# Kernel tuning notes

Measured on AMD Instinct MI355X. Metric: run time of the kernel, lower is better.

The kernel has to match this reference:

```python
import jax, jax.numpy as jnp
import numpy as np

N, E, B = 4096, 32768, 64
F_IN, E_FEAT, D, D3, G = 128, 64, 64, 64, 10
L = 3           # gc_count
SIG = 0.15      # prior_sig
LAMDA = 0.01    # DiffGroupNorm lambda
EPS = 1e-5      # BatchNorm eps


def setup_inputs() -> dict:
    key = jax.random.key(0)
    ks = jax.random.split(key, 24)
    u = lambda k, shape, s=0.02: jax.random.uniform(k, shape, jnp.float32, -s, s)
    return {
        "x": jax.random.normal(ks[0], (N, F_IN), jnp.float32),
        "edge_attr": jax.random.normal(ks[1], (E, E_FEAT), jnp.float32),
        "pre_W": u(ks[2], (F_IN, D)),
        "pre_b": u(ks[3], (D,)),
        "edge_w1": u(ks[4], (L, E_FEAT, D3), 0.1),
        "edge_b1": u(ks[5], (L, D3), 0.1),
        "edge_w2": u(ks[6], (L, D3, D * D), 0.05),
        "edge_b2": u(ks[7], (L, D * D), 0.05),
        "root_w": u(ks[8], (L, D, D), 0.1),
        "root_b": u(ks[9], (L, D), 0.1),
        "gru_wih": u(ks[10], (L, 3 * D, D), 0.1),
        "gru_whh": u(ks[11], (L, 3 * D, D), 0.1),
        "gru_bih": u(ks[12], (L, 3 * D), 0.1),
        "gru_bhh": u(ks[13], (L, 3 * D), 0.1),
        "gn_lin": u(ks[14], (L, D, G), 0.1),
        "gn_gamma": jnp.ones((L, G * D), jnp.float32),
        "gn_beta": jnp.zeros((L, G * D), jnp.float32),
        "post_W": u(ks[15], (D, D)),
        "post_b": u(ks[16], (D,)),
        "out_W": u(ks[17], (D, 1)),
        "out_b": u(ks[18], (1,)),
        "edge_index": jax.random.randint(ks[19], (2, E), 0, N),
        "batch": jnp.sort(jax.random.randint(ks[20], (N,), 0, B)),
    }


def _kld_det(W, b):
    # BayesLinear forward with sample=False: closed-form prior term
    logc = jnp.log(SIG * jnp.sqrt(2.0 * np.pi))
    return (0.5 * (W / SIG) ** 2 + logc).sum() + (0.5 * (b / SIG) ** 2 + logc).sum()


def _seg_mean(v, idx, num):
    s = jax.ops.segment_sum(v, idx, num_segments=num)
    c = jax.ops.segment_sum(jnp.ones((v.shape[0],), v.dtype), idx, num_segments=num)
    return s / jnp.clip(c, 1.0)[:, None]


def _gru_cell(m, h, wih, whh, bih, bhh):
    # torch GRU gate order: r, z, n
    gi = m @ wih.T + bih          # [N, 3D]
    gh = h @ whh.T + bhh
    i_r, i_z, i_n = jnp.split(gi, 3, axis=-1)
    h_r, h_z, h_n = jnp.split(gh, 3, axis=-1)
    r = jax.nn.sigmoid(i_r + h_r)
    z = jax.nn.sigmoid(i_z + h_z)
    n = jnp.tanh(i_n + r * h_n)
    return (1.0 - z) * n + z * h


def _diff_group_norm(m, lin, gamma, beta):
    # PyG DiffGroupNorm: x + lamda * sum_g s[:,g] * BN(s*x)
    s = jax.nn.softmax(m @ lin, axis=-1)           # [N, G]
    t = (s[:, :, None] * m[:, None, :]).reshape(m.shape[0], G * D)  # [N, G*D]
    mu = t.mean(axis=0)
    var = t.var(axis=0)                            # biased, as BatchNorm1d training
    tn = (t - mu) / jnp.sqrt(var + EPS) * gamma + beta
    return m + LAMDA * tn.reshape(m.shape[0], G, D).sum(axis=1)


def reference(x, edge_attr, pre_W, pre_b, edge_w1, edge_b1, edge_w2, edge_b2,
              root_w, root_b, gru_wih, gru_whh, gru_bih, gru_bhh,
              gn_lin, gn_gamma, gn_beta, post_W, post_b, out_W, out_b,
              edge_index, batch):
    src, dst = edge_index[0], edge_index[1]

    # pre FC (BayesLinear, sample=False) + relu
    out = jax.nn.relu(x @ pre_W + pre_b)
    tkl = _kld_det(pre_W, pre_b)
    prev = out
    h = out                                         # GRU hidden state

    for i in range(L):
        # edge-conditioned weights: MLP(edge_attr) -> [E, D, D]
        We = (jax.nn.relu(edge_attr @ edge_w1[i] + edge_b1[i]) @ edge_w2[i]
              + edge_b2[i]).reshape(E, D, D)
        msg = jnp.einsum('ef,efo->eo', out[src], We)        # gather + per-edge matmul
        agg = _seg_mean(msg, dst, N)                        # scatter-mean
        m = agg + out @ root_w[i] + root_b[i]               # NNConv root weight + bias
        m = _diff_group_norm(m, gn_lin[i], gn_gamma[i], gn_beta[i])
        m = jax.nn.relu(m)
        h = _gru_cell(m, h, gru_wih[i], gru_whh[i], gru_bih[i], gru_bhh[i])
        out = h + prev                                      # residual
        prev = out

    # early global_mean_pool over graphs
    pooled = _seg_mean(out, batch, B)                       # [B, D]
    p = jax.nn.relu(pooled @ post_W + post_b)
    tkl = tkl + _kld_det(post_W, post_b)
    y = p @ out_W + out_b                                   # [B, 1]
    tkl = tkl + _kld_det(out_W, out_b)
    return y.reshape(-1), tkl
```

## Files before the change

kernel.cpp:

```cpp
#include <hip/hip_runtime.h>
#include <math.h>

#define Nn 4096
#define Ee 32768
#define Bb 64
#define FINc 128
#define Dd 64
#define SIGf 0.15f
#define LAMf 0.01f
#define EPSf 1e-5f

typedef __attribute__((ext_vector_type(8))) short bf16x8;
typedef __attribute__((ext_vector_type(4))) float f32x4;

__device__ inline short f2bf(float f) {
  union { float f; unsigned u; } v; v.f = f;
  unsigned r = v.u + 0x7fffu + ((v.u >> 16) & 1u);
  return (short)(r >> 16);
}
__device__ inline bf16x8 pack8v(f32x4 a, f32x4 b) {
  bf16x8 r;
  r[0]=f2bf(a.x); r[1]=f2bf(a.y); r[2]=f2bf(a.z); r[3]=f2bf(a.w);
  r[4]=f2bf(b.x); r[5]=f2bf(b.y); r[6]=f2bf(b.z); r[7]=f2bf(b.w);
  return r;
}
__device__ inline float sigm(float x) { return 1.f / (1.f + expf(-x)); }

__global__ void k_tkl(const float* __restrict__ preW, const float* __restrict__ preb,
                      const float* __restrict__ postW, const float* __restrict__ postb,
                      const float* __restrict__ outW, const float* __restrict__ outb,
                      float* __restrict__ y) {
  int tid = threadIdx.x;
  const float logc = logf(SIGf * sqrtf(6.28318530717958647692f));
  const float c2 = 0.5f / (SIGf * SIGf);
  float acc = 0.f;
  for (int i = tid; i < FINc*Dd; i += 256) { float w = preW[i];  acc += c2*w*w + logc; }
  for (int i = tid; i < Dd; i += 256)      { float w = preb[i];  acc += c2*w*w + logc; }
  for (int i = tid; i < Dd*Dd; i += 256)   { float w = postW[i]; acc += c2*w*w + logc; }
  for (int i = tid; i < Dd; i += 256)      { float w = postb[i]; acc += c2*w*w + logc; }
  for (int i = tid; i < Dd; i += 256)      { float w = outW[i];  acc += c2*w*w + logc; }
  if (tid == 0)                            { float w = outb[0];  acc += c2*w*w + logc; }
  __shared__ float red[256];
  red[tid] = acc; __syncthreads();
  for (int s = 128; s > 0; s >>= 1) { if (tid < s) red[tid] += red[tid+s]; __syncthreads(); }
  if (tid == 0) y[Bb] = red[0];
}

__global__ void k_count(const int* __restrict__ dst, float* __restrict__ cnt) {
  int e = blockIdx.x * 256 + threadIdx.x;
  if (e < Ee) atomicAdd(&cnt[dst[e]], 1.0f);
}

__global__ void k_prep(const float* __restrict__ w1, const float* __restrict__ w2,
                       const float* __restrict__ b2, const float* __restrict__ rootw,
                       const float* __restrict__ gwih, const float* __restrict__ gwhh,
                       const float* __restrict__ preW,
                       short* __restrict__ w1T, short* __restrict__ b2T,
                       short* __restrict__ w2T, short* __restrict__ rootwT,
                       short* __restrict__ gwihB, short* __restrict__ gwhhB,
                       short* __restrict__ preWT) {
  int idx = blockIdx.x * 256 + threadIdx.x;
  if (idx < 3*64*64*64) {
    int f = idx & 63, o = (idx >> 6) & 63, h = (idx >> 12) & 63, l = idx >> 18;
    w2T[idx] = f2bf(w2[(((l*64 + h)*64 + f) << 6) + o]);
  }
  if (idx < 3*64*64) {
    int f = idx & 63, h = (idx >> 6) & 63, l = idx >> 12;
    w1T[idx] = f2bf(w1[l*4096 + f*64 + h]);
    b2T[idx] = f2bf(b2[l*4096 + f*64 + h]);
    rootwT[idx] = f2bf(rootw[l*4096 + f*64 + h]);
  }
  if (idx < 3*192*64) {
    gwihB[idx] = f2bf(gwih[idx]);
    gwhhB[idx] = f2bf(gwhh[idx]);
  }
  if (idx < 64*128) {
    int k = idx & 127, d = idx >> 7;
    preWT[idx] = f2bf(preW[k*64 + d]);
  }
}

__global__ __launch_bounds__(256) void k_pre(const float* __restrict__ x,
                                             const short* __restrict__ preWT,
                                             const float* __restrict__ preb,
                                             float* __restrict__ out, float* __restrict__ h) {
  const int tid = threadIdx.x, lane = tid & 63, wave = tid >> 6;
  const int m15 = lane & 15, kq = lane >> 4;
  const int nb = blockIdx.x * 32;
  const f32x4 zero4 = {0.f,0.f,0.f,0.f};
  const int d = wave*16 + m15;
  bf16x8 bfr[4];
  #pragma unroll
  for (int c = 0; c < 4; ++c)
    bfr[c] = *(const bf16x8*)(preWT + d*128 + c*32 + kq*8);
  #pragma unroll
  for (int t = 0; t < 2; ++t) {
    const float* xp = x + (size_t)(nb + t*16 + m15)*128 + kq*8;
    f32x4 p = zero4;
    #pragma unroll
    for (int c = 0; c < 4; ++c) {
      bf16x8 a = pack8v(*(const f32x4*)(xp + c*32), *(const f32x4*)(xp + c*32 + 4));
      p = __builtin_amdgcn_mfma_f32_16x16x32_bf16(a, bfr[c], p, 0, 0, 0);
    }
    float bv = preb[d];
    #pragma unroll
    for (int r = 0; r < 4; ++r) {
      int node = nb + t*16 + kq*4 + r;
      float v = fmaxf(p[r] + bv, 0.f);
      out[node*64 + d] = v;
      h[node*64 + d] = v;
    }
  }
}

__global__ __launch_bounds__(256) void k_msg(
    const float* __restrict__ out, const float* __restrict__ edge_attr,
    const short* __restrict__ w1T, const float* __restrict__ b1,
    const short* __restrict__ w2T, const short* __restrict__ b2T,
    const int* __restrict__ src, const int* __restrict__ dst,
    float* __restrict__ agg) {
  __shared__ __align__(16) float hidT[64*68];
  __shared__ int srcv[64];
  __shared__ int dstv[64];

  const int tid  = threadIdx.x;
  const int lane = tid & 63;
  const int wave = tid >> 6;
  const int m15  = lane & 15;
  const int kq   = lane >> 4;
  const int ebase = blockIdx.x * 64;

  if (tid < 64) { srcv[tid] = src[ebase + tid]; dstv[tid] = dst[ebase + tid]; }
  __syncthreads();

  const f32x4 zero4 = {0.f, 0.f, 0.f, 0.f};

  bf16x8 sfrag[4][2];
  #pragma unroll
  for (int t = 0; t < 4; ++t) {
    int node = srcv[t*16 + m15];
    const float* sp = out + node*64 + kq*8;
    #pragma unroll
    for (int ks = 0; ks < 2; ++ks) {
      f32x4 a = *(const f32x4*)(sp + ks*32);
      f32x4 b = *(const f32x4*)(sp + ks*32 + 4);
      sfrag[t][ks] = pack8v(a, b);
    }
  }

  {
    const short* wp = w1T + (wave*16 + m15)*64 + kq*8;
    bf16x8 bw0 = *(const bf16x8*)(wp);
    bf16x8 bw1 = *(const bf16x8*)(wp + 32);
    float b1v = b1[wave*16 + m15];
    #pragma unroll
    for (int t = 0; t < 4; ++t) {
      const float* ep = edge_attr + (size_t)(ebase + t*16 + m15)*64 + kq*8;
      bf16x8 a0 = pack8v(*(const f32x4*)(ep),      *(const f32x4*)(ep + 4));
      bf16x8 a1 = pack8v(*(const f32x4*)(ep + 32), *(const f32x4*)(ep + 36));
      f32x4 p = __builtin_amdgcn_mfma_f32_16x16x32_bf16(a0, bw0, zero4, 0, 0, 0);
      p = __builtin_amdgcn_mfma_f32_16x16x32_bf16(a1, bw1, p, 0, 0, 0);
      f32x4 v;
      v.x = fmaxf(p.x + b1v, 0.f); v.y = fmaxf(p.y + b1v, 0.f);
      v.z = fmaxf(p.z + b1v, 0.f); v.w = fmaxf(p.w + b1v, 0.f);
      *(f32x4*)(hidT + (wave*16 + m15)*68 + t*16 + kq*4) = v;
    }
  }
  __syncthreads();

  f32x4 acc[4] = {zero4, zero4, zero4, zero4};
  const short* w2base = w2T + (wave*16 + m15)*64 + kq*8;
  const short* b2base = b2T + (wave*16 + m15)*64 + kq*8;
  bf16x8 bc0 = *(const bf16x8*)(w2base);
  bf16x8 bc1 = *(const bf16x8*)(w2base + 32);
  for (int h = 0; h < 64; ++h) {
    const short* nb = (h < 63) ? (w2base + (h + 1)*4096) : b2base;
    bf16x8 pb0 = *(const bf16x8*)(nb);
    bf16x8 pb1 = *(const bf16x8*)(nb + 32);
    #pragma unroll
    for (int t = 0; t < 4; ++t) {
      f32x4 p = __builtin_amdgcn_mfma_f32_16x16x32_bf16(sfrag[t][0], bc0, zero4, 0, 0, 0);
      p = __builtin_amdgcn_mfma_f32_16x16x32_bf16(sfrag[t][1], bc1, p, 0, 0, 0);
      f32x4 hv = *(const f32x4*)(hidT + h*68 + t*16 + kq*4);
      acc[t].x += hv.x * p.x; acc[t].y += hv.y * p.y;
      acc[t].z += hv.z * p.z; acc[t].w += hv.w * p.w;
    }
    bc0 = pb0; bc1 = pb1;
  }
  #pragma unroll
  for (int t = 0; t < 4; ++t) {
    f32x4 p = __builtin_amdgcn_mfma_f32_16x16x32_bf16(sfrag[t][0], bc0, zero4, 0, 0, 0);
    p = __builtin_amdgcn_mfma_f32_16x16x32_bf16(sfrag[t][1], bc1, p, 0, 0, 0);
    acc[t].x += p.x; acc[t].y += p.y; acc[t].z += p.z; acc[t].w += p.w;
  }

  const int o = wave*16 + m15;
  #pragma unroll
  for (int t = 0; t < 4; ++t) {
    #pragma unroll
    for (int r = 0; r < 4; ++r) {
      int e = t*16 + kq*4 + r;
      atomicAdd(&agg[dstv[e]*64 + o], acc[t][r]);
    }
  }
}

__global__ __launch_bounds__(256) void k_m_fused(
    const float* __restrict__ agg, const float* __restrict__ cnt,
    const float* __restrict__ out, const short* __restrict__ rootwT,
    const float* __restrict__ rootb, const float* __restrict__ gnlin,
    float* __restrict__ m, float* __restrict__ sbuf, float* __restrict__ stats) {
  __shared__ float msh[64*65];
  __shared__ float lgsh[64*12];
  __shared__ float ssh[64*16];
  const int tid = threadIdx.x, lane = tid & 63, wave = tid >> 6;
  const int m15 = lane & 15, kq = lane >> 4;
  const int nb = blockIdx.x * 64;
  const f32x4 zero4 = {0.f,0.f,0.f,0.f};
  const int d = wave*16 + m15;

  bf16x8 b0 = *(const bf16x8*)(rootwT + d*64 + kq*8);
  bf16x8 b1 = *(const bf16x8*)(rootwT + d*64 + 32 + kq*8);
  float rbv = rootb[d];
  #pragma unroll
  for (int t = 0; t < 4; ++t) {
    const float* sp = out + (size_t)(nb + t*16 + m15)*64 + kq*8;
    bf16x8 a0 = pack8v(*(const f32x4*)(sp),      *(const f32x4*)(sp + 4));
    bf16x8 a1 = pack8v(*(const f32x4*)(sp + 32), *(const f32x4*)(sp + 36));
    f32x4 p = __builtin_amdgcn_mfma_f32_16x16x32_bf16(a0, b0, zero4, 0, 0, 0);
    p = __builtin_amdgcn_mfma_f32_16x16x32_bf16(a1, b1, p, 0, 0, 0);
    #pragma unroll
    for (int r = 0; r < 4; ++r) {
      int ln = t*16 + kq*4 + r;
      int node = nb + ln;
      float mv = agg[node*64 + d] / fmaxf(cnt[node], 1.f) + rbv + p[r];
      m[node*64 + d] = mv;
      msh[ln*65 + d] = mv;
    }
  }
  __syncthreads();

  for (int c = tid; c < 1024; c += 256) {
    int n = c >> 4, g = c & 15;
    if (g < 10) {
      float lg = 0.f;
      #pragma unroll 8
      for (int k = 0; k < 64; ++k) lg += msh[n*65 + k] * gnlin[k*10 + g];
      lgsh[n*12 + g] = lg;
    }
  }
  __syncthreads();
  for (int c = tid; c < 1024; c += 256) {
    int n = c >> 4, g = c & 15;
    if (g < 10) {
      float mx = -1e30f;
      #pragma unroll
      for (int gg = 0; gg < 10; ++gg) mx = fmaxf(mx, lgsh[n*12 + gg]);
      float sum = 0.f;
      #pragma unroll
      for (int gg = 0; gg < 10; ++gg) sum += expf(lgsh[n*12 + gg] - mx);
      float sv = expf(lgsh[n*12 + g] - mx) / sum;
      sbuf[(nb + n)*16 + g] = sv;
      ssh[n*16 + g] = sv;
    }
  }
  __syncthreads();
  for (int c = tid; c < 640; c += 256) {
    int g = c >> 6, dd = c & 63;
    float a1 = 0.f, a2 = 0.f;
    #pragma unroll 8
    for (int n = 0; n < 64; ++n) {
      float t = ssh[n*16 + g] * msh[n*65 + dd];
      a1 += t; a2 += t*t;
    }
    atomicAdd(&stats[c], a1);
    atomicAdd(&stats[640 + c], a2);
  }
}

__global__ __launch_bounds__(256) void k_gru(
    const float* __restrict__ m, const float* __restrict__ sbuf,
    const float* __restrict__ stats, const float* __restrict__ gamma,
    const float* __restrict__ beta, const short* __restrict__ gwihB,
    const short* __restrict__ gwhhB, const float* __restrict__ bih,
    const float* __restrict__ bhh, float* __restrict__ h,
    float* __restrict__ out) {
  __shared__ __align__(16) float mrsh[32*68];
  __shared__ float igsh[640];
  __shared__ float Bsh[64];
  __shared__ float ssh[512];
  const int tid = threadIdx.x, lane = tid & 63, wave = tid >> 6;
  const int m15 = lane & 15, kq = lane >> 4;
  const int nb = blockIdx.x * 32;
  const f32x4 zero4 = {0.f,0.f,0.f,0.f};
  const float invN = 1.f / (float)Nn;

  if (tid < 64) {
    float bacc = 0.f;
    #pragma unroll
    for (int g = 0; g < 10; ++g) {
      int c = g*64 + tid;
      float mu = stats[c] * invN;
      float var = stats[640 + c] * invN - mu*mu;
      float ig = (1.0f / sqrtf(var + EPSf)) * gamma[c];
      igsh[c] = ig;
      bacc += beta[c] - mu * ig;
    }
    Bsh[tid] = bacc;
  }
  if (tid < 512) ssh[tid] = sbuf[nb*16 + tid];
  __syncthreads();

  for (int idx = tid; idx < 2048; idx += 256) {
    int n = idx >> 6, dd = idx & 63;
    float mv = m[(nb + n)*64 + dd];
    float SA = 0.f;
    #pragma unroll
    for (int g = 0; g < 10; ++g) SA += ssh[n*16 + g] * igsh[g*64 + dd];
    mrsh[n*68 + dd] = fmaxf(mv * (1.f + LAMf*SA) + LAMf*Bsh[dd], 0.f);
  }
  __syncthreads();

  bf16x8 mrf[2][2], hf[2][2];
  #pragma unroll
  for (int t = 0; t < 2; ++t) {
    const float* mp = mrsh + (t*16 + m15)*68 + kq*8;
    const float* hp = h + (size_t)(nb + t*16 + m15)*64 + kq*8;
    #pragma unroll
    for (int ks = 0; ks < 2; ++ks) {
      mrf[t][ks] = pack8v(*(const f32x4*)(mp + ks*32), *(const f32x4*)(mp + ks*32 + 4));
      hf[t][ks]  = pack8v(*(const f32x4*)(hp + ks*32), *(const f32x4*)(hp + ks*32 + 4));
    }
  }
  const int d = wave*16 + m15;
  f32x4 gi[2][3], gh[2][3];
  #pragma unroll
  for (int p = 0; p < 3; ++p) {
    int j = p*64 + d;
    bf16x8 bi0 = *(const bf16x8*)(gwihB + j*64 + kq*8);
    bf16x8 bi1 = *(const bf16x8*)(gwihB + j*64 + 32 + kq*8);
    bf16x8 bh0 = *(const bf16x8*)(gwhhB + j*64 + kq*8);
    bf16x8 bh1 = *(const bf16x8*)(gwhhB + j*64 + 32 + kq*8);
    #pragma unroll
    for (int t = 0; t < 2; ++t) {
      f32x4 a = __builtin_amdgcn_mfma_f32_16x16x32_bf16(mrf[t][0], bi0, zero4, 0, 0, 0);
      gi[t][p] = __builtin_amdgcn_mfma_f32_16x16x32_bf16(mrf[t][1], bi1, a, 0, 0, 0);
      f32x4 b = __builtin_amdgcn_mfma_f32_16x16x32_bf16(hf[t][0], bh0, zero4, 0, 0, 0);
      gh[t][p] = __builtin_amdgcn_mfma_f32_16x16x32_bf16(hf[t][1], bh1, b, 0, 0, 0);
    }
  }
  float bir = bih[d],      bhr = bhh[d];
  float biz = bih[64 + d], bhz = bhh[64 + d];
  float bin = bih[128 + d], bhn = bhh[128 + d];
  __syncthreads();
  #pragma unroll
  for (int t = 0; t < 2; ++t) {
    #pragma unroll
    for (int r = 0; r < 4; ++r) {
      int node = nb + t*16 + kq*4 + r;
      float rr = sigm(gi[t][0][r] + bir + gh[t][0][r] + bhr);
      float z  = sigm(gi[t][1][r] + biz + gh[t][1][r] + bhz);
      float nn = tanhf(gi[t][2][r] + bin + rr * (gh[t][2][r] + bhn));
      float hv = h[node*64 + d];
      float hn = (1.f - z) * nn + z * hv;
      h[node*64 + d] = hn;
      out[node*64 + d] = hn + out[node*64 + d];
    }
  }
}

__global__ void k_pool(const float* __restrict__ out, const int* __restrict__ batch,
                       float* __restrict__ pooled, float* __restrict__ pcnt) {
  int idx = blockIdx.x * 256 + threadIdx.x;
  int n = idx >> 6, d = idx & 63;
  int b = batch[n];
  atomicAdd(&pooled[b*64 + d], out[idx]);
  if (d == 0) atomicAdd(&pcnt[b], 1.f);
}

__global__ void k_final(const float* __restrict__ pooled, const float* __restrict__ pcnt,
                        const float* __restrict__ postW, const float* __restrict__ postb,
                        const float* __restrict__ outW, const float* __restrict__ outb,
                        float* __restrict__ y) {
  int b = blockIdx.x, d = threadIdx.x;
  __shared__ float pl[64];
  float c = fmaxf(pcnt[b], 1.f);
  pl[d] = pooled[b*64 + d] / c;
  __syncthreads();
  float acc = postb[d];
  #pragma unroll 8
  for (int k = 0; k < 64; ++k) acc += pl[k] * postW[k*64 + d];
  acc = fmaxf(acc, 0.f);
  float v = acc * outW[d];
  #pragma unroll
  for (int off = 32; off > 0; off >>= 1) v += __shfl_down(v, off, 64);
  if (d == 0) y[b] = v + outb[0];
}

extern "C" void kernel_launch(void* const* d_in, const int* in_sizes, int n_in,
                              void* d_out, int out_size, void* d_ws, size_t ws_size,
                              hipStream_t stream) {
  (void)in_sizes; (void)n_in; (void)out_size; (void)ws_size;
  const float* x        = (const float*)d_in[0];
  const float* edge_attr= (const float*)d_in[1];
  const float* preW     = (const float*)d_in[2];
  const float* preb     = (const float*)d_in[3];
  const float* ew1      = (const float*)d_in[4];
  const float* eb1      = (const float*)d_in[5];
  const float* ew2      = (const float*)d_in[6];
  const float* eb2      = (const float*)d_in[7];
  const float* rootw    = (const float*)d_in[8];
  const float* rootb    = (const float*)d_in[9];
  const float* gwih     = (const float*)d_in[10];
  const float* gwhh     = (const float*)d_in[11];
  const float* gbih     = (const float*)d_in[12];
  const float* gbhh     = (const float*)d_in[13];
  const float* gnlin    = (const float*)d_in[14];
  const float* gngamma  = (const float*)d_in[15];
  const float* gnbeta   = (const float*)d_in[16];
  const float* postW    = (const float*)d_in[17];
  const float* postb    = (const float*)d_in[18];
  const float* outW     = (const float*)d_in[19];
  const float* outb     = (const float*)d_in[20];
  const int*   eidx     = (const int*)d_in[21];
  const int*   batch    = (const int*)d_in[22];
  const int* src = eidx;
  const int* dst = eidx + Ee;
  float* y = (float*)d_out;

  float* ws     = (float*)d_ws;
  float* out    = ws;
  float* hbuf   = out    + Nn*64;
  float* mbuf   = hbuf   + Nn*64;
  float* sbuf   = mbuf   + Nn*64;
  float* agg    = sbuf   + Nn*16;
  float* stats  = agg    + Nn*64;
  float* cnt    = stats  + 2048;
  float* pooled = cnt    + Nn;
  float* pcnt   = pooled + Nn;
  float* bfbase = pcnt   + 64;
  short* w1T    = (short*)bfbase;
  short* b2T    = w1T    + 3*4096;
  short* w2T    = b2T    + 3*4096;
  short* rootwT = w2T    + 3*262144;
  short* gwihB  = rootwT + 3*4096;
  short* gwhhB  = gwihB  + 3*12288;
  short* preWT  = gwhhB  + 3*12288;

  hipMemsetAsync(cnt, 0, (Nn + Nn + 64)*sizeof(float), stream);

  k_prep<<<3072, 256, 0, stream>>>(ew1, ew2, eb2, rootw, gwih, gwhh, preW,
                                   w1T, b2T, w2T, rootwT, gwihB, gwhhB, preWT);
  k_tkl<<<1, 256, 0, stream>>>(preW, preb, postW, postb, outW, outb, y);
  k_count<<<Ee/256, 256, 0, stream>>>(dst, cnt);
  k_pre<<<Nn/32, 256, 0, stream>>>(x, preWT, preb, out, hbuf);

  for (int i = 0; i < 3; ++i) {
    hipMemsetAsync(agg, 0, (Nn*64 + 2048)*sizeof(float), stream);
    k_msg<<<Ee/64, 256, 0, stream>>>(out, edge_attr,
                                     w1T + i*4096, eb1 + i*64,
                                     w2T + i*262144, b2T + i*4096,
                                     src, dst, agg);
    k_m_fused<<<Nn/64, 256, 0, stream>>>(agg, cnt, out, rootwT + i*4096,
                                         rootb + i*64, gnlin + i*640, mbuf, sbuf, stats);
    k_gru<<<Nn/32, 256, 0, stream>>>(mbuf, sbuf, stats, gngamma + i*640, gnbeta + i*640,
                                     gwihB + i*12288, gwhhB + i*12288,
                                     gbih + i*192, gbhh + i*192, hbuf, out);
  }

  k_pool<<<Nn*64/256, 256, 0, stream>>>(out, batch, pooled, pcnt);
  k_final<<<Bb, 64, 0, stream>>>(pooled, pcnt, postW, postb, outW, outb, y);
}
```

Baseline: 379.1 us.

## Merge setup kernels, split k_msg hidden loop across waves, fuse pool and zeroing

Folds weight conversion, KL term, edge/pool counting into one k_setup launch, with w2 transposed through shared memory for coalescing. k_msg now uses 512 threads: two wave groups each process half of the 64 hidden units and reduce through LDS before the atomics, doubling wave parallelism per block. The per-layer agg memset is replaced by zeroing agg inside k_m_fused after it is read, stats get per-layer slices, and the global mean pool atomics are fused into the last k_gru. These cut launch count and memset overhead and raise occupancy in the dominant message kernel, at the cost of extra LDS reduction and syncs.

```diff
diff --git a/kernel.cpp b/kernel.cpp
--- a/kernel.cpp
+++ b/kernel.cpp
@@ -26,57 +26,73 @@
 }
 __device__ inline float sigm(float x) { return 1.f / (1.f + expf(-x)); }
 
-__global__ void k_tkl(const float* __restrict__ preW, const float* __restrict__ preb,
-                      const float* __restrict__ postW, const float* __restrict__ postb,
-                      const float* __restrict__ outW, const float* __restrict__ outb,
-                      float* __restrict__ y) {
-  int tid = threadIdx.x;
-  const float logc = logf(SIGf * sqrtf(6.28318530717958647692f));
-  const float c2 = 0.5f / (SIGf * SIGf);
-  float acc = 0.f;
-  for (int i = tid; i < FINc*Dd; i += 256) { float w = preW[i];  acc += c2*w*w + logc; }
-  for (int i = tid; i < Dd; i += 256)      { float w = preb[i];  acc += c2*w*w + logc; }
-  for (int i = tid; i < Dd*Dd; i += 256)   { float w = postW[i]; acc += c2*w*w + logc; }
-  for (int i = tid; i < Dd; i += 256)      { float w = postb[i]; acc += c2*w*w + logc; }
-  for (int i = tid; i < Dd; i += 256)      { float w = outW[i];  acc += c2*w*w + logc; }
-  if (tid == 0)                            { float w = outb[0];  acc += c2*w*w + logc; }
-  __shared__ float red[256];
-  red[tid] = acc; __syncthreads();
-  for (int s = 128; s > 0; s >>= 1) { if (tid < s) red[tid] += red[tid+s]; __syncthreads(); }
-  if (tid == 0) y[Bb] = red[0];
-}
-
-__global__ void k_count(const int* __restrict__ dst, float* __restrict__ cnt) {
-  int e = blockIdx.x * 256 + threadIdx.x;
-  if (e < Ee) atomicAdd(&cnt[dst[e]], 1.0f);
-}
-
-__global__ void k_prep(const float* __restrict__ w1, const float* __restrict__ w2,
-                       const float* __restrict__ b2, const float* __restrict__ rootw,
-                       const float* __restrict__ gwih, const float* __restrict__ gwhh,
-                       const float* __restrict__ preW,
-                       short* __restrict__ w1T, short* __restrict__ b2T,
-                       short* __restrict__ w2T, short* __restrict__ rootwT,
-                       short* __restrict__ gwihB, short* __restrict__ gwhhB,
-                       short* __restrict__ preWT) {
-  int idx = blockIdx.x * 256 + threadIdx.x;
-  if (idx < 3*64*64*64) {
-    int f = idx & 63, o = (idx >> 6) & 63, h = (idx >> 12) & 63, l = idx >> 18;
-    w2T[idx] = f2bf(w2[(((l*64 + h)*64 + f) << 6) + o]);
-  }
-  if (idx < 3*64*64) {
-    int f = idx & 63, h = (idx >> 6) & 63, l = idx >> 12;
-    w1T[idx] = f2bf(w1[l*4096 + f*64 + h]);
-    b2T[idx] = f2bf(b2[l*4096 + f*64 + h]);
-    rootwT[idx] = f2bf(rootw[l*4096 + f*64 + h]);
-  }
-  if (idx < 3*192*64) {
-    gwihB[idx] = f2bf(gwih[idx]);
-    gwhhB[idx] = f2bf(gwhh[idx]);
-  }
-  if (idx < 64*128) {
-    int k = idx & 127, d = idx >> 7;
-    preWT[idx] = f2bf(preW[k*64 + d]);
+__global__ __launch_bounds__(256) void k_setup(
+    const float* __restrict__ w1, const float* __restrict__ w2,
+    const float* __restrict__ b2, const float* __restrict__ rootw,
+    const float* __restrict__ gwih, const float* __restrict__ gwhh,
+    const float* __restrict__ preW,
+    const float* __restrict__ preb, const float* __restrict__ postW,
+    const float* __restrict__ postb, const float* __restrict__ outW,
+    const float* __restrict__ outb,
+    const int* __restrict__ dst, const int* __restrict__ batch,
+    short* __restrict__ w1T, short* __restrict__ b2T,
+    short* __restrict__ w2T, short* __restrict__ rootwT,
+    short* __restrict__ gwihB, short* __restrict__ gwhhB,
+    short* __restrict__ preWT,
+    float* __restrict__ cnt, float* __restrict__ pcnt, float* __restrict__ y) {
+  const int b = blockIdx.x, tid = threadIdx.x;
+  if (b < 192) {
+    __shared__ float tile[64*65];
+    const int l = b >> 6, h = b & 63;
+    const float* srcp = w2 + (size_t)(l*64 + h)*4096;
+    #pragma unroll
+    for (int it = 0; it < 16; ++it) {
+      int j = tid + 256*it;
+      tile[(j >> 6)*65 + (j & 63)] = srcp[j];
+    }
+    __syncthreads();
+    short* dstp = w2T + (size_t)(l*64 + h)*4096;
+    #pragma unroll
+    for (int it = 0; it < 16; ++it) {
+      int j = tid + 256*it;
+      int o = j >> 6, f = j & 63;
+      dstp[j] = f2bf(tile[f*65 + o]);
+    }
+  } else if (b < 200) {
+    int base = (b - 192)*256 + tid;
+    for (int idx = base; idx < 12288; idx += 2048) {
+      int l = idx >> 12, r = idx & 4095;
+      int f = r & 63, c = r >> 6;
+      w1T[idx]    = f2bf(w1[l*4096 + f*64 + c]);
+      b2T[idx]    = f2bf(b2[l*4096 + f*64 + c]);
+      rootwT[idx] = f2bf(rootw[l*4096 + f*64 + c]);
+    }
+    for (int idx = base; idx < 36864; idx += 2048) {
+      gwihB[idx] = f2bf(gwih[idx]);
+      gwhhB[idx] = f2bf(gwhh[idx]);
+    }
+    for (int idx = base; idx < 8192; idx += 2048) {
+      int k = idx & 127, d = idx >> 7;
+      preWT[idx] = f2bf(preW[k*64 + d]);
+    }
+  } else if (b < 328) {
+    int e = (b - 200)*256 + tid;
+    atomicAdd(&cnt[dst[e]], 1.0f);
+    if (e < Nn) atomicAdd(&pcnt[batch[e]], 1.0f);
+  } else {
+    const float logc = logf(SIGf * sqrtf(6.28318530717958647692f));
+    const float c2 = 0.5f / (SIGf * SIGf);
+    float acc = 0.f;
+    for (int i = tid; i < FINc*Dd; i += 256) { float w = preW[i];  acc += c2*w*w + logc; }
+    for (int i = tid; i < Dd; i += 256)      { float w = preb[i];  acc += c2*w*w + logc; }
+    for (int i = tid; i < Dd*Dd; i += 256)   { float w = postW[i]; acc += c2*w*w + logc; }
+    for (int i = tid; i < Dd; i += 256)      { float w = postb[i]; acc += c2*w*w + logc; }
+    for (int i = tid; i < Dd; i += 256)      { float w = outW[i];  acc += c2*w*w + logc; }
+    if (tid == 0)                            { float w = outb[0];  acc += c2*w*w + logc; }
+    __shared__ float red[256];
+    red[tid] = acc; __syncthreads();
+    for (int s = 128; s > 0; s >>= 1) { if (tid < s) red[tid] += red[tid+s]; __syncthreads(); }
+    if (tid == 0) y[Bb] = red[0];
   }
 }
 
@@ -113,7 +129,7 @@
   }
 }
 
-__global__ __launch_bounds__(256) void k_msg(
+__global__ __launch_bounds__(512, 4) void k_msg(
     const float* __restrict__ out, const float* __restrict__ edge_attr,
     const short* __restrict__ w1T, const float* __restrict__ b1,
     const short* __restrict__ w2T, const short* __restrict__ b2T,
@@ -125,7 +141,9 @@
 
   const int tid  = threadIdx.x;
   const int lane = tid & 63;
-  const int wave = tid >> 6;
+  const int w    = tid >> 6;
+  const int ow   = w & 3;
+  const int hh   = w >> 2;
   const int m15  = lane & 15;
   const int kq   = lane >> 4;
   const int ebase = blockIdx.x * 64;
@@ -139,22 +157,20 @@
   #pragma unroll
   for (int t = 0; t < 4; ++t) {
     int node = srcv[t*16 + m15];
-    const float* sp = out + node*64 + kq*8;
-    #pragma unroll
-    for (int ks = 0; ks < 2; ++ks) {
-      f32x4 a = *(const f32x4*)(sp + ks*32);
-      f32x4 b = *(const f32x4*)(sp + ks*32 + 4);
-      sfrag[t][ks] = pack8v(a, b);
-    }
+    const float* sp = out + (size_t)node*64 + kq*8;
+    #pragma unroll
+    for (int ks = 0; ks < 2; ++ks)
+      sfrag[t][ks] = pack8v(*(const f32x4*)(sp + ks*32), *(const f32x4*)(sp + ks*32 + 4));
   }
 
   {
-    const short* wp = w1T + (wave*16 + m15)*64 + kq*8;
+    const short* wp = w1T + (ow*16 + m15)*64 + kq*8;
     bf16x8 bw0 = *(const bf16x8*)(wp);
     bf16x8 bw1 = *(const bf16x8*)(wp + 32);
-    float b1v = b1[wave*16 + m15];
-    #pragma unroll
-    for (int t = 0; t < 4; ++t) {
+    float b1v = b1[ow*16 + m15];
+    #pragma unroll
+    for (int tt = 0; tt < 2; ++tt) {
+      int t = hh*2 + tt;
       const float* ep = edge_attr + (size_t)(ebase + t*16 + m15)*64 + kq*8;
       bf16x8 a0 = pack8v(*(const f32x4*)(ep),      *(const f32x4*)(ep + 4));
       bf16x8 a1 = pack8v(*(const f32x4*)(ep + 32), *(const f32x4*)(ep + 36));
@@ -163,53 +179,71 @@
       f32x4 v;
       v.x = fmaxf(p.x + b1v, 0.f); v.y = fmaxf(p.y + b1v, 0.f);
       v.z = fmaxf(p.z + b1v, 0.f); v.w = fmaxf(p.w + b1v, 0.f);
-      *(f32x4*)(hidT + (wave*16 + m15)*68 + t*16 + kq*4) = v;
+      *(f32x4*)(hidT + (ow*16 + m15)*68 + t*16 + kq*4) = v;
     }
   }
   __syncthreads();
 
   f32x4 acc[4] = {zero4, zero4, zero4, zero4};
-  const short* w2base = w2T + (wave*16 + m15)*64 + kq*8;
-  const short* b2base = b2T + (wave*16 + m15)*64 + kq*8;
-  bf16x8 bc0 = *(const bf16x8*)(w2base);
-  bf16x8 bc1 = *(const bf16x8*)(w2base + 32);
-  for (int h = 0; h < 64; ++h) {
-    const short* nb = (h < 63) ? (w2base + (h + 1)*4096) : b2base;
-    bf16x8 pb0 = *(const bf16x8*)(nb);
-    bf16x8 pb1 = *(const bf16x8*)(nb + 32);
+  const short* base = w2T + (ow*16 + m15)*64 + kq*8;
+  const short* b2p  = b2T + (ow*16 + m15)*64 + kq*8;
+  const short* p0 = base + (size_t)(hh*32)*4096;
+  const short* p1 = base + (size_t)(hh*32 + 1)*4096;
+  bf16x8 c00 = *(const bf16x8*)p0, c01 = *(const bf16x8*)(p0 + 32);
+  bf16x8 c10 = *(const bf16x8*)p1, c11 = *(const bf16x8*)(p1 + 32);
+  for (int c = 0; c < 32; ++c) {
+    const short* pn = (c < 30) ? base + (size_t)(hh*32 + c + 2)*4096 : b2p;
+    bf16x8 n0 = *(const bf16x8*)pn, n1 = *(const bf16x8*)(pn + 32);
     #pragma unroll
     for (int t = 0; t < 4; ++t) {
-      f32x4 p = __builtin_amdgcn_mfma_f32_16x16x32_bf16(sfrag[t][0], bc0, zero4, 0, 0, 0);
-      p = __builtin_amdgcn_mfma_f32_16x16x32_bf16(sfrag[t][1], bc1, p, 0, 0, 0);
-      f32x4 hv = *(const f32x4*)(hidT + h*68 + t*16 + kq*4);
+      f32x4 p = __builtin_amdgcn_mfma_f32_16x16x32_bf16(sfrag[t][0], c00, zero4, 0, 0, 0);
+      p = __builtin_amdgcn_mfma_f32_16x16x32_bf16(sfrag[t][1], c01, p, 0, 0, 0);
+      f32x4 hv = *(const f32x4*)(hidT + (hh*32 + c)*68 + t*16 + kq*4);
       acc[t].x += hv.x * p.x; acc[t].y += hv.y * p.y;
       acc[t].z += hv.z * p.z; acc[t].w += hv.w * p.w;
     }
-    bc0 = pb0; bc1 = pb1;
-  }
-  #pragma unroll
-  for (int t = 0; t < 4; ++t) {
-    f32x4 p = __builtin_amdgcn_mfma_f32_16x16x32_bf16(sfrag[t][0], bc0, zero4, 0, 0, 0);
-    p = __builtin_amdgcn_mfma_f32_16x16x32_bf16(sfrag[t][1], bc1, p, 0, 0, 0);
-    acc[t].x += p.x; acc[t].y += p.y; acc[t].z += p.z; acc[t].w += p.w;
-  }
-
-  const int o = wave*16 + m15;
-  #pragma unroll
-  for (int t = 0; t < 4; ++t) {
-    #pragma unroll
-    for (int r = 0; r < 4; ++r) {
-      int e = t*16 + kq*4 + r;
-      atomicAdd(&agg[dstv[e]*64 + o], acc[t][r]);
+    c00 = c10; c01 = c11; c10 = n0; c11 = n1;
+  }
+  if (hh) {
+    #pragma unroll
+    for (int t = 0; t < 4; ++t) {
+      f32x4 p = __builtin_amdgcn_mfma_f32_16x16x32_bf16(sfrag[t][0], c00, zero4, 0, 0, 0);
+      p = __builtin_amdgcn_mfma_f32_16x16x32_bf16(sfrag[t][1], c01, p, 0, 0, 0);
+      acc[t].x += p.x; acc[t].y += p.y; acc[t].z += p.z; acc[t].w += p.w;
+    }
+  }
+
+  __syncthreads();
+  if (hh) {
+    #pragma unroll
+    for (int t = 0; t < 4; ++t)
+      *(f32x4*)(hidT + (ow*64 + lane)*17 + t*4) = acc[t];
+  }
+  __syncthreads();
+  if (!hh) {
+    #pragma unroll
+    for (int t = 0; t < 4; ++t) {
+      f32x4 o4 = *(const f32x4*)(hidT + (ow*64 + lane)*17 + t*4);
+      acc[t].x += o4.x; acc[t].y += o4.y; acc[t].z += o4.z; acc[t].w += o4.w;
+    }
+    const int o = ow*16 + m15;
+    #pragma unroll
+    for (int t = 0; t < 4; ++t) {
+      #pragma unroll
+      for (int r = 0; r < 4; ++r) {
+        int e = t*16 + kq*4 + r;
+        atomicAdd(&agg[(size_t)dstv[e]*64 + o], acc[t][r]);
+      }
     }
   }
 }
 
 __global__ __launch_bounds__(256) void k_m_fused(
-    const float* __restrict__ agg, const float* __restrict__ cnt,
+    const float* __restrict__ agg_c, const float* __restrict__ cnt,
     const float* __restrict__ out, const short* __restrict__ rootwT,
     const float* __restrict__ rootb, const float* __restrict__ gnlin,
-    float* __restrict__ m, float* __restrict__ sbuf, float* __restrict__ stats) {
+    float* __restrict__ m, float* __restrict__ sbuf, float* __restrict__ stats,
+    float* __restrict__ agg_z) {
   __shared__ float msh[64*65];
   __shared__ float lgsh[64*12];
   __shared__ float ssh[64*16];
@@ -233,7 +267,8 @@
     for (int r = 0; r < 4; ++r) {
       int ln = t*16 + kq*4 + r;
       int node = nb + ln;
-      float mv = agg[node*64 + d] / fmaxf(cnt[node], 1.f) + rbv + p[r];
+      float mv = agg_c[node*64 + d] / fmaxf(cnt[node], 1.f) + rbv + p[r];
+      agg_z[node*64 + d] = 0.f;
       m[node*64 + d] = mv;
       msh[ln*65 + d] = mv;
     }
@@ -284,7 +319,8 @@
     const float* __restrict__ beta, const short* __restrict__ gwihB,
     const short* __restrict__ gwhhB, const float* __restrict__ bih,
     const float* __restrict__ bhh, float* __restrict__ h,
-    float* __restrict__ out) {
+    float* __restrict__ out, const int* __restrict__ batch,
+    float* __restrict__ pooled, int do_pool) {
   __shared__ __align__(16) float mrsh[32*68];
   __shared__ float igsh[640];
   __shared__ float Bsh[64];
@@ -364,18 +400,11 @@
       float hv = h[node*64 + d];
       float hn = (1.f - z) * nn + z * hv;
       h[node*64 + d] = hn;
-      out[node*64 + d] = hn + out[node*64 + d];
-    }
-  }
-}
-
-__global__ void k_pool(const float* __restrict__ out, const int* __restrict__ batch,
-                       float* __restrict__ pooled, float* __restrict__ pcnt) {
-  int idx = blockIdx.x * 256 + threadIdx.x;
-  int n = idx >> 6, d = idx & 63;
-  int b = batch[n];
-  atomicAdd(&pooled[b*64 + d], out[idx]);
-  if (d == 0) atomicAdd(&pcnt[b], 1.f);
+      float ov = hn + out[node*64 + d];
+      out[node*64 + d] = ov;
+      if (do_pool) atomicAdd(&pooled[batch[node]*64 + d], ov);
+    }
+  }
 }
 
 __global__ void k_final(const float* __restrict__ pooled, const float* __restrict__ pcnt,
@@ -435,9 +464,9 @@
   float* sbuf   = mbuf   + Nn*64;
   float* agg    = sbuf   + Nn*16;
   float* stats  = agg    + Nn*64;
-  float* cnt    = stats  + 2048;
+  float* cnt    = stats  + 3*2048;
   float* pooled = cnt    + Nn;
-  float* pcnt   = pooled + Nn;
+  float* pcnt   = pooled + 4096;
   float* bfbase = pcnt   + 64;
   short* w1T    = (short*)bfbase;
   short* b2T    = w1T    + 3*4096;
@@ -447,27 +476,30 @@
   short* gwhhB  = gwihB  + 3*12288;
   short* preWT  = gwhhB  + 3*12288;
 
-  hipMemsetAsync(cnt, 0, (Nn + Nn + 64)*sizeof(float), stream);
-
-  k_prep<<<3072, 256, 0, stream>>>(ew1, ew2, eb2, rootw, gwih, gwhh, preW,
-                                   w1T, b2T, w2T, rootwT, gwihB, gwhhB, preWT);
-  k_tkl<<<1, 256, 0, stream>>>(preW, preb, postW, postb, outW, outb, y);
-  k_count<<<Ee/256, 256, 0, stream>>>(dst, cnt);
+  size_t zfloats = (size_t)Nn*64 + 3*2048 + Nn + 4096 + 64;
+  hipMemsetAsync(agg, 0, zfloats*sizeof(float), stream);
+
+  k_setup<<<329, 256, 0, stream>>>(ew1, ew2, eb2, rootw, gwih, gwhh, preW,
+                                   preb, postW, postb, outW, outb,
+                                   dst, batch,
+                                   w1T, b2T, w2T, rootwT, gwihB, gwhhB, preWT,
+                                   cnt, pcnt, y);
   k_pre<<<Nn/32, 256, 0, stream>>>(x, preWT, preb, out, hbuf);
 
   for (int i = 0; i < 3; ++i) {
-    hipMemsetAsync(agg, 0, (Nn*64 + 2048)*sizeof(float), stream);
-    k_msg<<<Ee/64, 256, 0, stream>>>(out, edge_attr,
+    k_msg<<<Ee/64, 512, 0, stream>>>(out, edge_attr,
                                      w1T + i*4096, eb1 + i*64,
                                      w2T + i*262144, b2T + i*4096,
                                      src, dst, agg);
     k_m_fused<<<Nn/64, 256, 0, stream>>>(agg, cnt, out, rootwT + i*4096,
-                                         rootb + i*64, gnlin + i*640, mbuf, sbuf, stats);
-    k_gru<<<Nn/32, 256, 0, stream>>>(mbuf, sbuf, stats, gngamma + i*640, gnbeta + i*640,
+                                         rootb + i*64, gnlin + i*640, mbuf, sbuf,
+                                         stats + i*2048, agg);
+    k_gru<<<Nn/32, 256, 0, stream>>>(mbuf, sbuf, stats + i*2048,
+                                     gngamma + i*640, gnbeta + i*640,
                                      gwihB + i*12288, gwhhB + i*12288,
-                                     gbih + i*192, gbhh + i*192, hbuf, out);
-  }
-
-  k_pool<<<Nn*64/256, 256, 0, stream>>>(out, batch, pooled, pcnt);
+                                     gbih + i*192, gbhh + i*192, hbuf, out,
+                                     batch, pooled, (i == 2) ? 1 : 0);
+  }
+
   k_final<<<Bb, 64, 0, stream>>>(pooled, pcnt, postW, postb, outW, outb, y);
 }
```

Result: slower. 519.1 us (+36.9%).
